# Performance work log

Measured on AMD Instinct MI355X. Metric: run time of the kernel, lower is better.

## Reference

```python
import jax, jax.numpy as jnp
import numpy as np

B, T, S, L, R, H, UE = 64, 256, 16, 128, 16, 256, 64


def setup_inputs() -> dict:
    key = jax.random.key(0)
    ks = jax.random.split(key, 10)
    u = jax.random.normal(ks[0], (B, T, UE), jnp.float32)
    k = 0.1 * jax.random.normal(ks[1], (B, T, L), jnp.float32)
    K = 0.1 * jax.random.normal(ks[2], (B, T, L, R), jnp.float32)
    eps_z = jax.random.normal(ks[3], (T, S, B, L), jnp.float32)
    eps_w = jax.random.normal(ks[4], (T, S, B, R), jnp.float32)
    W1 = jax.random.normal(ks[5], (L, H), jnp.float32) / np.sqrt(L).astype(np.float32)
    W2 = jax.random.normal(ks[6], (H, L), jnp.float32) / np.sqrt(H).astype(np.float32)
    m_init = jax.random.normal(ks[7], (L,), jnp.float32)
    Q_diag = jax.random.uniform(ks[8], (L,), jnp.float32, 0.1, 1.0)
    Q0_diag = jax.random.uniform(ks[9], (L,), jnp.float32, 0.5, 1.5)
    return dict(u=u, k=k, K=K, eps_z=eps_z, eps_w=eps_w, W1=W1, W2=W2,
                m_init=m_init, Q_diag=Q_diag, Q0_diag=Q0_diag, n_samples=S)


def reference(u, k, K, eps_z, eps_w, W1, W2, m_init, Q_diag, Q0_diag, n_samples):
    Bn, Tn, Ln, Rn = K.shape
    ue = u.shape[-1]
    I_r = jnp.eye(Rn, dtype=K.dtype)

    def bmv(A, x):      # A: [B,L,R], x: [...,B,R] -> [...,B,L]
        return jnp.einsum('blr,...br->...bl', A, x)

    def bmvT(A, x):     # A: [B,L,R], x: [...,B,L] -> [...,B,R]
        return jnp.einsum('blr,...bl->...br', A, x)

    def mean_fn(z):
        return z + jnp.tanh(z @ W1) @ W2

    def step_core(m, K_t, k_t, ez, ew, q_a):
        # A = I + K^T diag(q_a) K  (rank x rank)
        A = I_r + jnp.einsum('blr,l,blq->brq', K_t, q_a, K_t)
        Lc = jnp.linalg.cholesky(A)
        Linv = jax.scipy.linalg.solve_triangular(
            Lc, jnp.broadcast_to(I_r, Lc.shape), lower=True)

        def csolve(x):  # solve A y = x via Linv^T Linv x
            y = jnp.einsum('bij,...bj->...bi', Linv, x)
            return jnp.einsum('bji,...bj->...bi', Linv, y)

        # gain direction; inner shift always uses Q_diag (as in torch source)
        g = k_t - bmv(K_t, csolve(bmvT(K_t, m + Q_diag * k_t)))
        m_f = m + q_a * g
        z_p = jnp.sqrt(q_a) * ez
        z_f = m_f + z_p - bmv(K_t, csolve(bmvT(K_t, z_p) + ew))
        qp = jnp.sum(q_a * g * g, axis=-1)
        M = A - I_r  # = K^T diag(q_a) K
        tr = -jnp.einsum('bij,bjk,bik->b', Linv, M, Linv)
        logdet = 2.0 * jnp.sum(jnp.log(jnp.diagonal(Lc, axis1=-2, axis2=-1)), axis=-1)
        kl = 0.5 * (qp + tr + logdet)
        return z_f, m_f, z_p, kl

    # ---- t = 0 (uses initial covariance Q0_diag) ----
    m0 = jnp.broadcast_to(m_init, (Bn, Ln))
    m0 = m0.at[:, :ue].add(u[:, 0])
    z_f0, m_f0, z_p0, kl0 = step_core(m0, K[:, 0], k[:, 0], eps_z[0], eps_w[0], Q0_diag)

    # ---- t = 1..T-1: sequential nonlinear filter scan ----
    def scan_fn(z_prev, xs):
        u_t, k_t, K_t, ez, ew = xs
        m = mean_fn(z_prev)            # [S,B,L]
        m = m.at[..., :ue].add(u_t)    # broadcast input over samples
        z_f, m_f, z_p, kl = step_core(m, K_t, k_t, ez, ew, Q_diag)
        return z_f, (z_f, m_f.mean(axis=0), z_p, kl.mean(axis=0))

    xs = (jnp.swapaxes(u[:, 1:], 0, 1),
          jnp.swapaxes(k[:, 1:], 0, 1),
          jnp.swapaxes(K[:, 1:], 0, 1),
          eps_z[1:], eps_w[1:])
    _, (z_fs, m_fs, z_ps, kls) = jax.lax.scan(scan_fn, z_f0, xs)

    z_f = jnp.transpose(jnp.concatenate([z_f0[None], z_fs], 0), (1, 2, 0, 3))  # [S,B,T,L]
    m_f = jnp.transpose(jnp.concatenate([m_f0[None], m_fs], 0), (1, 0, 2))     # [B,T,L]
    z_p = jnp.transpose(jnp.concatenate([z_p0[None], z_ps], 0), (1, 2, 0, 3))  # [S,B,T,L]
    kl = jnp.concatenate([kl0[None], kls], 0).T                                 # [B,T]
    return z_f, m_f, z_p, kl
```

## Files before the change

kernel.cpp:

```cpp
#include <hip/hip_runtime.h>
#include <cstddef>

typedef _Float16 half8v __attribute__((ext_vector_type(8)));
typedef _Float16 half4v __attribute__((ext_vector_type(4)));
typedef float f32x4 __attribute__((ext_vector_type(4)));

#define MFMA32(A, B, C) __builtin_amdgcn_mfma_f32_16x16x32_f16(A, B, C, 0, 0, 0)
#define MFMA16(A, B, C) __builtin_amdgcn_mfma_f32_16x16x16f16(A, B, C, 0, 0, 0)

__global__ void kw2_kernel(const float* __restrict__ W2, _Float16* __restrict__ w2h) {
  int i = blockIdx.x * 256 + threadIdx.x;
  w2h[i] = (_Float16)W2[i];
}

__global__ void kprep1_kernel(const float* __restrict__ Kg,
                              const float* __restrict__ kg,
                              const float* __restrict__ ug,
                              const float* __restrict__ Qd,
                              const float* __restrict__ Q0d,
                              float* __restrict__ Ainv,
                              float* __restrict__ klc,
                              _Float16* __restrict__ pfb,
                              float* __restrict__ cgp) {
  int tid = threadIdx.x;
  int wv = tid >> 6, ln = tid & 63;
  size_t bt = (size_t)blockIdx.x * 4 + wv;
  int t = (int)(bt & 255);
  __shared__ float Ks[4][128][20];
  __shared__ float qs[4][128];
  __shared__ float vvs[4][128];
  __shared__ float Asm[4][16][20];
  __shared__ float LiL[4][16][20];
  __shared__ float AiS[4][16][20];
  __shared__ float yps[4][4][16];
  __shared__ float yvs[4][16];

  const float* kp = Kg + bt * 2048;
  for (int i = ln; i < 2048; i += 64) Ks[wv][i >> 4][i & 15] = kp[i];
  for (int l = ln; l < 128; l += 64) {
    float q = (t == 0) ? Q0d[l] : Qd[l];
    qs[wv][l] = q;
    float v = Qd[l] * kg[bt * 128 + l];
    if (t > 0 && l < 64) v += ug[bt * 64 + l];
    vvs[wv][l] = v;
  }
  __syncthreads();
  {
    int r = ln & 15, c0 = (ln >> 4) << 2;
    float a0 = 0, a1 = 0, a2 = 0, a3 = 0;
    for (int l = 0; l < 128; ++l) {
      float kq = Ks[wv][l][r] * qs[wv][l];
      const float* row = &Ks[wv][l][c0];
      a0 += kq * row[0]; a1 += kq * row[1]; a2 += kq * row[2]; a3 += kq * row[3];
    }
    Asm[wv][r][c0 + 0] = a0 + ((r == c0 + 0) ? 1.f : 0.f);
    Asm[wv][r][c0 + 1] = a1 + ((r == c0 + 1) ? 1.f : 0.f);
    Asm[wv][r][c0 + 2] = a2 + ((r == c0 + 2) ? 1.f : 0.f);
    Asm[wv][r][c0 + 3] = a3 + ((r == c0 + 3) ? 1.f : 0.f);
  }
  {
    int r = ln & 15, seg = ln >> 4;
    float s = 0.f;
    for (int l = seg * 32; l < seg * 32 + 32; ++l) s += Ks[wv][l][r] * vvs[wv][l];
    yps[wv][seg][r] = s;
  }
  __syncthreads();
  if (ln < 16) {
    int i = ln;
    float ar[16], Lr[16];
#pragma unroll
    for (int j = 0; j < 16; ++j) ar[j] = Asm[wv][i][j];
    float ld = 0.f;
#pragma unroll
    for (int j = 0; j < 16; ++j) {
      float ajj = __shfl(ar[j], j, 64);
      float d = sqrtf(ajj);
      ld += __logf(d);
      float li = ar[j] / d;
      li = (i >= j) ? li : 0.f;
      Lr[j] = li;
#pragma unroll
      for (int k2 = j; k2 < 16; ++k2) {
        float lk = __shfl(li, k2, 64);
        ar[k2] -= li * lk;
      }
    }
    int cc = i;
    float Lic[16];
#pragma unroll
    for (int ii = 0; ii < 16; ++ii) {
      float s = (ii == cc) ? 1.f : 0.f;
#pragma unroll
      for (int p = 0; p < 16; ++p) {
        if (p < ii) {
          float Lip = __shfl(Lr[p], ii, 64);
          s -= Lip * Lic[p];
        }
      }
      float dii = __shfl(Lr[ii], ii, 64);
      float v = s / dii;
      Lic[ii] = (ii >= cc) ? v : 0.f;
    }
    float tr = 0.f;
#pragma unroll
    for (int ii = 0; ii < 16; ++ii) { tr += Lic[ii] * Lic[ii]; LiL[wv][cc][ii] = Lic[ii]; }
    tr += __shfl_xor(tr, 1); tr += __shfl_xor(tr, 2);
    tr += __shfl_xor(tr, 4); tr += __shfl_xor(tr, 8);
    if (cc == 0) klc[bt] = 0.5f * (tr - 16.f + 2.f * ld);
    yvs[wv][cc] = yps[wv][0][cc] + yps[wv][1][cc] + yps[wv][2][cc] + yps[wv][3][cc];
  }
  __syncthreads();
  {
    int r = ln & 15, c0 = (ln >> 4) << 2;
    float a0 = 0, a1 = 0, a2 = 0, a3 = 0;
    for (int ii = 0; ii < 16; ++ii) {
      float lir = LiL[wv][r][ii];
      a0 += lir * LiL[wv][c0 + 0][ii];
      a1 += lir * LiL[wv][c0 + 1][ii];
      a2 += lir * LiL[wv][c0 + 2][ii];
      a3 += lir * LiL[wv][c0 + 3][ii];
    }
    AiS[wv][r][c0 + 0] = a0; AiS[wv][r][c0 + 1] = a1;
    AiS[wv][r][c0 + 2] = a2; AiS[wv][r][c0 + 3] = a3;
    f32x4 av = {a0, a1, a2, a3};
    *(f32x4*)&Ainv[bt * 256 + r * 16 + c0] = av;
  }
  __syncthreads();
  {
#pragma unroll
    for (int li = 0; li < 2; ++li) {
      int l = ln * 2 + li;
      f32x4 acc0 = {0,0,0,0}, acc1v = {0,0,0,0}, acc2v = {0,0,0,0}, acc3v = {0,0,0,0};
      for (int j = 0; j < 16; ++j) {
        float kj = Ks[wv][l][j];
        acc0  += kj * *(const f32x4*)&AiS[wv][j][0];
        acc1v += kj * *(const f32x4*)&AiS[wv][j][4];
        acc2v += kj * *(const f32x4*)&AiS[wv][j][8];
        acc3v += kj * *(const f32x4*)&AiS[wv][j][12];
      }
      float ql = qs[wv][l];
      float cp = ql * kg[bt * 128 + l];
      float pv[16];
#pragma unroll
      for (int e = 0; e < 4; ++e) {
        pv[e] = ql * acc0[e]; pv[4 + e] = ql * acc1v[e];
        pv[8 + e] = ql * acc2v[e]; pv[12 + e] = ql * acc3v[e];
      }
#pragma unroll
      for (int r = 0; r < 16; ++r) cp -= pv[r] * yvs[wv][r];
      cgp[bt * 128 + l] = cp;
#pragma unroll
      for (int r = 0; r < 16; ++r) Ks[wv][l][r] = pv[r];
    }
  }
  __syncthreads();
  {
    int gp = ln >> 4, cp = ln & 15;
#pragma unroll
    for (int ci = 0; ci < 4; ++ci) {
      half8v o;
#pragma unroll
      for (int mt = 0; mt < 2; ++mt)
#pragma unroll
        for (int j = 0; j < 4; ++j)
          o[mt * 4 + j] = (_Float16)Ks[wv][ci * 32 + mt * 16 + cp][gp * 4 + j];
      *(half8v*)(pfb + bt * 2048 + (size_t)(ci * 64 + ln) * 8) = o;
    }
  }
}

__global__ void kprepR_kernel(const float* __restrict__ Kg,
                              const _Float16* __restrict__ w2h,
                              _Float16* __restrict__ rfb,
                              _Float16* __restrict__ kab) {
  int tid = threadIdx.x;
  int wv = tid >> 6, ln = tid & 63;
  int g = ln >> 4, c = ln & 15;
  __shared__ _Float16 Kh[128][20];
  __shared__ _Float16 Rh[16][264];
  for (int it = 0; it < 4; ++it) {
    size_t bt = (size_t)blockIdx.x * 4 + it;
    const float* kp = Kg + bt * 2048;
    for (int i = tid; i < 2048; i += 256) Kh[i >> 4][i & 15] = (_Float16)kp[i];
    __syncthreads();
    half8v kA[4];
#pragma unroll
    for (int kt = 0; kt < 4; ++kt)
#pragma unroll
      for (int j = 0; j < 8; ++j) kA[kt][j] = Kh[kt * 32 + g * 8 + j][c];
#pragma unroll
    for (int i = 0; i < 4; ++i) {
      int tile = wv * 4 + i;
      f32x4 acc = {0, 0, 0, 0};
#pragma unroll
      for (int kt = 0; kt < 4; ++kt) {
        half8v bf = *(const half8v*)&w2h[(size_t)(tile * 16 + c) * 128 + kt * 32 + g * 8];
        acc = MFMA32(kA[kt], bf, acc);
      }
#pragma unroll
      for (int r = 0; r < 4; ++r) Rh[g * 4 + r][tile * 16 + c] = (_Float16)acc[r];
    }
    __syncthreads();
    half8v r0, r1;
#pragma unroll
    for (int mt = 0; mt < 4; ++mt)
#pragma unroll
      for (int j = 0; j < 4; ++j) {
        _Float16 v = Rh[c][wv * 64 + mt * 16 + g * 4 + j];
        if (mt < 2) r0[mt * 4 + j] = v; else r1[(mt - 2) * 4 + j] = v;
      }
    *(half8v*)(rfb + bt * 4096 + (size_t)tid * 16) = r0;
    *(half8v*)(rfb + bt * 4096 + (size_t)tid * 16 + 8) = r1;
    if (kab) {
      half8v ko;
#pragma unroll
      for (int kt = 0; kt < 2; ++kt)
#pragma unroll
        for (int j = 0; j < 4; ++j) ko[kt * 4 + j] = Kh[wv * 32 + kt * 16 + g * 4 + j][c];
      *(half8v*)(kab + bt * 2048 + (size_t)tid * 8) = ko;
    }
    __syncthreads();
  }
}

__global__ void kc_kernel(const float* __restrict__ Kg,
                          const float* __restrict__ epsz,
                          const float* __restrict__ epsw,
                          const float* __restrict__ Qd,
                          const float* __restrict__ Q0d,
                          const float* __restrict__ Ainv,
                          float* __restrict__ out_zf,
                          float* __restrict__ out_zp,
                          float* __restrict__ zpcb,
                          int zw, int wzp) {
  int idx = blockIdx.x;
  int t = idx >> 6, b = idx & 63;
  int bt = b * 256 + t;
  __shared__ float Ks[128][16];
  __shared__ float Ai[16][16];
  __shared__ float zp[16][129];
  __shared__ float hh[16][17];
  __shared__ float ww[16][17];
  __shared__ float sq[128];
  const float* kp = Kg + (size_t)bt * 2048;
  for (int i = threadIdx.x; i < 2048; i += 256) ((float*)Ks)[i] = kp[i];
  ((float*)Ai)[threadIdx.x] = Ainv[(size_t)bt * 256 + threadIdx.x];
  const float* q = (t == 0) ? Q0d : Qd;
  if (threadIdx.x < 128) sq[threadIdx.x] = sqrtf(q[threadIdx.x]);
  __syncthreads();
  for (int i = threadIdx.x; i < 2048; i += 256) {
    int s = i >> 7, l = i & 127;
    float v = sq[l] * epsz[(((size_t)t * 16 + s) * 64 + b) * 128 + l];
    zp[s][l] = v;
    if (wzp) out_zp[(((size_t)s * 64 + b) * 256 + t) * 128 + l] = v;
  }
  __syncthreads();
  {
    int s = threadIdx.x >> 4, r = threadIdx.x & 15;
    float acc = epsw[(((size_t)t * 16 + s) * 64 + b) * 16 + r];
    for (int l = 0; l < 128; ++l) acc += Ks[l][r] * zp[s][l];
    hh[s][r] = acc;
  }
  __syncthreads();
  {
    int s = threadIdx.x >> 4, r = threadIdx.x & 15;
    float acc = 0.f;
    for (int j = 0; j < 16; ++j) acc += Ai[r][j] * hh[s][j];
    ww[s][r] = acc;
  }
  __syncthreads();
  for (int i = threadIdx.x; i < 2048; i += 256) {
    int s = i >> 7, l = i & 127;
    float acc = 0.f;
    for (int r = 0; r < 16; ++r) acc += Ks[l][r] * ww[s][r];
    float v = zp[s][l] - acc;
    if (zw) zpcb[(size_t)bt * 2048 + i] = v;
    else out_zf[(((size_t)s * 64 + b) * 256 + t) * 128 + l] = v;
  }
}

__global__ void kzp_kernel(const float* __restrict__ epsz,
                           const float* __restrict__ Qd,
                           const float* __restrict__ Q0d,
                           float* __restrict__ out_zp) {
  for (size_t i = (size_t)blockIdx.x * blockDim.x + threadIdx.x; i < (size_t)33554432;
       i += (size_t)gridDim.x * blockDim.x) {
    int l = (int)(i & 127);
    int t = (int)((i >> 7) & 255);
    int sb = (int)(i >> 15);
    int s = sb >> 6, b = sb & 63;
    float q = (t == 0) ? Q0d[l] : Qd[l];
    out_zp[i] = sqrtf(q) * epsz[(((size_t)t * 16 + s) * 64 + b) * 128 + l];
  }
}

#define BAR() asm volatile("s_waitcnt lgkmcnt(0)\n\ts_barrier" ::: "memory")

template <bool PK, bool ZW>
__device__ __forceinline__ void scan_body(
    const int b, const int ct,
    _Float16* __restrict__ svhc, _Float16* __restrict__ hbc,
    float (*__restrict__ h2pc)[320], float (*__restrict__ qppc)[64],
    const float* __restrict__ ug, const float* __restrict__ Kg,
    const float* __restrict__ W1, const float* __restrict__ W2,
    const float* __restrict__ m_init, const float* __restrict__ Qd,
    const float* __restrict__ Q0d, const _Float16* __restrict__ pfb,
    const float* __restrict__ cgp, const _Float16* __restrict__ rfb,
    const _Float16* __restrict__ kab, const float* __restrict__ zpcb,
    const float* __restrict__ klcp, float* __restrict__ out_zf,
    float* __restrict__ out_mf, float* __restrict__ out_kl) {
  const int wvc = ct >> 6;
  const int ln = ct & 63;
  const int g = ln >> 4;
  const int c = ln & 15;

  half8v w1f[4][4];
#pragma unroll
  for (int mt = 0; mt < 4; ++mt)
#pragma unroll
    for (int kt = 0; kt < 4; ++kt) {
      half8v v;
#pragma unroll
      for (int j = 0; j < 8; ++j)
        v[j] = (_Float16)W1[(size_t)(kt * 32 + g * 8 + j) * 256 + (wvc * 64 + mt * 16 + c)];
      w1f[mt][kt] = v;
    }
  half8v w2f[2][8];
#pragma unroll
  for (int mt = 0; mt < 2; ++mt)
#pragma unroll
    for (int kt = 0; kt < 8; ++kt) {
      half8v v;
#pragma unroll
      for (int j = 0; j < 8; ++j)
        v[j] = (_Float16)W2[(size_t)(kt * 32 + g * 8 + j) * 128 + (wvc * 32 + mt * 16 + c)];
      w2f[mt][kt] = v;
    }

  f32x4 qiv[2], qiv0[2];
#pragma unroll
  for (int mt = 0; mt < 2; ++mt) {
    f32x4 q = *(const f32x4*)&Qd[wvc * 32 + mt * 16 + g * 4];
    f32x4 q0 = *(const f32x4*)&Q0d[wvc * 32 + mt * 16 + g * 4];
#pragma unroll
    for (int r = 0; r < 4; ++r) { qiv[mt][r] = 1.f / q[r]; qiv0[mt][r] = 1.f / q0[r]; }
  }

  f32x4 zreg[2];

  half8v pfx0, pfx1, kax0 = {}, kax1 = {}, rfa0, rfa1, rfc0, rfc1;
  float kf0[8], kf1[8];
  f32x4 zq0[2], zq1[2], cv0[2], cv1[2];
  f32x4 ur0[2] = {}, ur1[2] = {};
  float kv0 = 0.f, kv1 = 0.f;

  const char* pf_p = (const char*)pfb + (size_t)b * 256 * 4096 + (size_t)ct * 16;
  const char* ka_p = PK ? (const char*)kab + (size_t)b * 256 * 4096 + (size_t)ct * 16
                        : (const char*)pfb;
  const char* K_p = (const char*)Kg + (size_t)b * 256 * 8192 + (size_t)((wvc * 32 + g * 4) * 16 + c) * 4;
  const char* rf_p = (const char*)rfb + (size_t)b * 256 * 8192 + (size_t)ct * 32;
  const char* zq_p = ZW ? (const char*)zpcb + (size_t)b * 256 * 8192 + (size_t)(c * 128 + wvc * 32 + g * 4) * 4
                        : (const char*)out_zf + ((((size_t)c * 64 + b) * 256) * 128 + wvc * 32 + g * 4) * 4;
  const size_t zq_str = ZW ? 8192 : 512;
  const char* cv_p = (const char*)cgp + (size_t)b * 256 * 512 + (size_t)(wvc * 32 + g * 4) * 4;
  const char* ur_p = (const char*)ug + (size_t)b * 256 * 256 + (size_t)(wvc * 32 + g * 4) * 4;
  const char* kl_p = (const char*)klcp + (size_t)b * 256 * 4;
  char* zf_p = (char*)out_zf + ((((size_t)c * 64 + b) * 256) * 128 + wvc * 32 + g * 4) * 4;
  char* mf_p = (char*)out_mf + ((size_t)b * 256 * 128 + wvc * 32 + g * 4) * 4;

#define STAGE(BI) do { \
    pfx##BI = *(const half8v*)pf_p; pf_p += 4096; \
    if constexpr (PK) { kax##BI = *(const half8v*)ka_p; ka_p += 4096; } \
    else { _Pragma("unroll") for (int kt_ = 0; kt_ < 2; ++kt_) \
             _Pragma("unroll") for (int j_ = 0; j_ < 4; ++j_) \
               kf##BI[kt_ * 4 + j_] = *(const float*)(K_p + kt_ * 1024 + j_ * 64); \
           K_p += 8192; } \
// ... 113 lines not shown
      v_ += __shfl_xor(v_, 4); v_ += __shfl_xor(v_, 8); \
      if (ct == 0) out_kl[(size_t)b * 256 + (size_t)(TPREV)] = 0.03125f * v_ + kv##PBI; \
    } \
  } while (0)

  STAGE(0);
  STAGE(1);
  {
    f32x4 mv0[2];
#pragma unroll
    for (int mt = 0; mt < 2; ++mt) {
      mv0[mt] = *(const f32x4*)&m_init[wvc * 32 + mt * 16 + g * 4];
      if (wvc < 2) mv0[mt] += ur0[mt];
    }
    half4v mh0[2], ml0[2];
#pragma unroll
    for (int kt = 0; kt < 2; ++kt)
#pragma unroll
      for (int j = 0; j < 4; ++j) {
        float x = mv0[kt][j];
        _Float16 h = (_Float16)x;
        mh0[kt][j] = h;
        ml0[kt][j] = (_Float16)(x - (float)h);
      }
    half4v ka0_, ka1_;
    KAH(0, 0, ka0_); KAH(0, 1, ka1_);
    f32x4 hz = {0, 0, 0, 0};
    hz = MFMA16(ka0_, mh0[0], hz); hz = MFMA16(ka1_, mh0[1], hz);
    hz = MFMA16(ka0_, ml0[0], hz); hz = MFMA16(ka1_, ml0[1], hz);
    *(f32x4*)&h2pc[wvc][c * 20 + g * 4] = hz;
    BAR();
    EPILOG(0, qiv0, mv0);
    BAR();
  }

  for (int t = 1; t < 255; t += 2) {
    KL_FIN(0, t - 1);
    STAGE(0);
    PHASE_A(1);
    BAR();
    PHASE_B(1, qiv);
    BAR();
    KL_FIN(1, t);
    STAGE(1);
    PHASE_A(0);
    BAR();
    PHASE_B(0, qiv);
    BAR();
  }
  KL_FIN(0, 254);
  PHASE_A(1);
  BAR();
  PHASE_B(1, qiv);
  BAR();
  KL_FIN(1, 255);

#undef STAGE
#undef KAH
#undef PHASE_A
#undef EPILOG
#undef PHASE_B
#undef KL_FIN
}

template <bool PK, bool ZW>
__launch_bounds__(256, 1)
__global__ void kscan1_kernel(const float* __restrict__ ug, const float* __restrict__ Kg,
                              const float* __restrict__ W1, const float* __restrict__ W2,
                              const float* __restrict__ m_init, const float* __restrict__ Qd,
                              const float* __restrict__ Q0d, const _Float16* __restrict__ pfb,
                              const float* __restrict__ cgp, const _Float16* __restrict__ rfb,
                              const _Float16* __restrict__ kab, const float* __restrict__ zpcb,
                              const float* __restrict__ klcp, float* __restrict__ out_zf,
                              float* __restrict__ out_mf, float* __restrict__ out_kl) {
  __shared__ __align__(16) _Float16 svh[2048];
  __shared__ __align__(16) _Float16 hb[4096];
  __shared__ float h2p[4][320];
  __shared__ float qpp[2][64];
  scan_body<PK, ZW>(blockIdx.x, threadIdx.x, svh, hb, h2p, qpp,
                    ug, Kg, W1, W2, m_init, Qd, Q0d, pfb, cgp, rfb, kab, zpcb, klcp,
                    out_zf, out_mf, out_kl);
}

template <bool PK, bool ZW>
__attribute__((amdgpu_flat_work_group_size(512, 512)))
__attribute__((amdgpu_waves_per_eu(2, 2)))
__global__ void kscan2_kernel(const float* __restrict__ ug, const float* __restrict__ Kg,
                              const float* __restrict__ W1, const float* __restrict__ W2,
                              const float* __restrict__ m_init, const float* __restrict__ Qd,
                              const float* __restrict__ Q0d, const _Float16* __restrict__ pfb,
                              const float* __restrict__ cgp, const _Float16* __restrict__ rfb,
                              const _Float16* __restrict__ kab, const float* __restrict__ zpcb,
                              const float* __restrict__ klcp, float* __restrict__ out_zf,
                              float* __restrict__ out_mf, float* __restrict__ out_kl) {
  __shared__ __align__(16) _Float16 svh[2][2048];
  __shared__ __align__(16) _Float16 hb[2][4096];
  __shared__ float h2p[2][4][320];
  __shared__ float qpp[2][2][64];
  const int ch = threadIdx.x >> 8;
  scan_body<PK, ZW>(blockIdx.x * 2 + ch, threadIdx.x & 255,
                    svh[ch], hb[ch], h2p[ch], qpp[ch],
                    ug, Kg, W1, W2, m_init, Qd, Q0d, pfb, cgp, rfb, kab, zpcb, klcp,
                    out_zf, out_mf, out_kl);
}

extern "C" void kernel_launch(void* const* d_in, const int* in_sizes, int n_in,
                              void* d_out, int out_size, void* d_ws, size_t ws_size,
                              hipStream_t stream) {
  (void)in_sizes; (void)n_in; (void)out_size;
  const float* u   = (const float*)d_in[0];
  const float* kk  = (const float*)d_in[1];
  const float* Kg  = (const float*)d_in[2];
  const float* epz = (const float*)d_in[3];
  const float* epw = (const float*)d_in[4];
  const float* W1  = (const float*)d_in[5];
  const float* W2  = (const float*)d_in[6];
  const float* mi  = (const float*)d_in[7];
  const float* Qd  = (const float*)d_in[8];
  const float* Q0d = (const float*)d_in[9];

  float* out_zf = (float*)d_out;
  float* out_mf = out_zf + (size_t)33554432;
  float* out_zp = out_mf + (size_t)2097152;
  float* out_kl = out_zp + (size_t)33554432;

  char* ws = (char*)d_ws;
  size_t off = 0;
  auto take = [&](size_t n) { char* p = ws + off; off += n; return p; };
  float*    Ainv = (float*)take(16777216);
  float*    klc  = (float*)take(65536);
  float*    cgp  = (float*)take(8388608);
  _Float16* pfb  = (_Float16*)take(67108864);
  _Float16* w2h  = (_Float16*)take(65536);
  bool zw = ws_size >= off + 134217728;
  float* zpcb = zw ? (float*)take(134217728) : nullptr;
  bool pk = zw && (ws_size >= off + 67108864);
  _Float16* kab = pk ? (_Float16*)take(67108864) : nullptr;
  bool rfws = ws_size >= off + 134217728;
  _Float16* rfb = rfws ? (_Float16*)take(134217728) : (_Float16*)out_zp;
  int wzp = rfws ? 1 : 0;

  kw2_kernel<<<128, 256, 0, stream>>>(W2, w2h);
  kprep1_kernel<<<4096, 256, 0, stream>>>(Kg, kk, u, Qd, Q0d, Ainv, klc, pfb, cgp);
  kprepR_kernel<<<4096, 256, 0, stream>>>(Kg, w2h, rfb, kab);
  kc_kernel<<<16384, 256, 0, stream>>>(Kg, epz, epw, Qd, Q0d, Ainv, out_zf, out_zp,
                                       zpcb, zw ? 1 : 0, wzp);

  auto pick = [&](const void* f2) {
    hipFuncAttributes fa;
    if (hipFuncGetAttributes(&fa, f2) == hipSuccess)
      return fa.localSizeBytes == 0 && fa.numRegs > 140;
    return false;
  };
#define LAUNCH_SCAN(PKV, ZWV) do { \
    if (pick((const void*)kscan2_kernel<PKV, ZWV>)) \
      kscan2_kernel<PKV, ZWV><<<32, 512, 0, stream>>>(u, Kg, W1, W2, mi, Qd, Q0d, pfb, cgp, rfb, kab, zpcb, klc, out_zf, out_mf, out_kl); \
    else \
      kscan1_kernel<PKV, ZWV><<<64, 256, 0, stream>>>(u, Kg, W1, W2, mi, Qd, Q0d, pfb, cgp, rfb, kab, zpcb, klc, out_zf, out_mf, out_kl); \
  } while (0)

  if (pk)      LAUNCH_SCAN(true,  true);
  else if (zw) LAUNCH_SCAN(false, true);
  else         LAUNCH_SCAN(false, false);
#undef LAUNCH_SCAN

  if (!rfws) kzp_kernel<<<2048, 256, 0, stream>>>(epz, Qd, Q0d, out_zp);
}
```

Before: 1.078 ms.

## Fuse R-factor precompute into correction kernel and drop two-chain scan variant

Adds a kc2 kernel that computes the fp16 K·W2 R-factors and fp16 K copy inside the same per-(b,t) block that computes the noise correction, so K is read from global memory once instead of twice. Introduces a fixed workspace layout path when the workspace is large enough, always writing z_p directly and launching the single-chain kscan1 scan. Removes the runtime attribute-based selection of the 512-thread two-chain scan kernel. The trade-off is a heavier fused kernel with more shared memory and fewer parallel blocks per CU, plus losing the kscan2 variant if it was the one being picked.

```diff
diff --git a/kernel.cpp b/kernel.cpp
--- a/kernel.cpp
+++ b/kernel.cpp
@@ -11,287 +11,6 @@
 __global__ void kw2_kernel(const float* __restrict__ W2, _Float16* __restrict__ w2h) {
   int i = blockIdx.x * 256 + threadIdx.x;
   w2h[i] = (_Float16)W2[i];
-}
-
-__global__ void kprep1_kernel(const float* __restrict__ Kg,
-                              const float* __restrict__ kg,
-                              const float* __restrict__ ug,
-                              const float* __restrict__ Qd,
-                              const float* __restrict__ Q0d,
-                              float* __restrict__ Ainv,
-                              float* __restrict__ klc,
-                              _Float16* __restrict__ pfb,
-                              float* __restrict__ cgp) {
-  int tid = threadIdx.x;
-  int wv = tid >> 6, ln = tid & 63;
-  size_t bt = (size_t)blockIdx.x * 4 + wv;
-  int t = (int)(bt & 255);
-  __shared__ float Ks[4][128][20];
-  __shared__ float qs[4][128];
-  __shared__ float vvs[4][128];
-  __shared__ float Asm[4][16][20];
-  __shared__ float LiL[4][16][20];
-  __shared__ float AiS[4][16][20];
-  __shared__ float yps[4][4][16];
-  __shared__ float yvs[4][16];
-
-  const float* kp = Kg + bt * 2048;
-  for (int i = ln; i < 2048; i += 64) Ks[wv][i >> 4][i & 15] = kp[i];
-  for (int l = ln; l < 128; l += 64) {
-    float q = (t == 0) ? Q0d[l] : Qd[l];
-    qs[wv][l] = q;
-    float v = Qd[l] * kg[bt * 128 + l];
-    if (t > 0 && l < 64) v += ug[bt * 64 + l];
-    vvs[wv][l] = v;
-  }
-  __syncthreads();
-  {
-    int r = ln & 15, c0 = (ln >> 4) << 2;
-    float a0 = 0, a1 = 0, a2 = 0, a3 = 0;
-    for (int l = 0; l < 128; ++l) {
-      float kq = Ks[wv][l][r] * qs[wv][l];
-      const float* row = &Ks[wv][l][c0];
-      a0 += kq * row[0]; a1 += kq * row[1]; a2 += kq * row[2]; a3 += kq * row[3];
-    }
-    Asm[wv][r][c0 + 0] = a0 + ((r == c0 + 0) ? 1.f : 0.f);
-    Asm[wv][r][c0 + 1] = a1 + ((r == c0 + 1) ? 1.f : 0.f);
-    Asm[wv][r][c0 + 2] = a2 + ((r == c0 + 2) ? 1.f : 0.f);
-    Asm[wv][r][c0 + 3] = a3 + ((r == c0 + 3) ? 1.f : 0.f);
-  }
-  {
-    int r = ln & 15, seg = ln >> 4;
-    float s = 0.f;
-    for (int l = seg * 32; l < seg * 32 + 32; ++l) s += Ks[wv][l][r] * vvs[wv][l];
-    yps[wv][seg][r] = s;
-  }
-  __syncthreads();
-  if (ln < 16) {
-    int i = ln;
-    float ar[16], Lr[16];
-#pragma unroll
-    for (int j = 0; j < 16; ++j) ar[j] = Asm[wv][i][j];
-    float ld = 0.f;
-#pragma unroll
-    for (int j = 0; j < 16; ++j) {
-      float ajj = __shfl(ar[j], j, 64);
-      float d = sqrtf(ajj);
-      ld += __logf(d);
-      float li = ar[j] / d;
-      li = (i >= j) ? li : 0.f;
-      Lr[j] = li;
-#pragma unroll
-      for (int k2 = j; k2 < 16; ++k2) {
-        float lk = __shfl(li, k2, 64);
-        ar[k2] -= li * lk;
-      }
-    }
-    int cc = i;
-    float Lic[16];
-#pragma unroll
-    for (int ii = 0; ii < 16; ++ii) {
-      float s = (ii == cc) ? 1.f : 0.f;
-#pragma unroll
-      for (int p = 0; p < 16; ++p) {
-        if (p < ii) {
-          float Lip = __shfl(Lr[p], ii, 64);
-          s -= Lip * Lic[p];
-        }
-      }
-      float dii = __shfl(Lr[ii], ii, 64);
-      float v = s / dii;
-      Lic[ii] = (ii >= cc) ? v : 0.f;
-    }
-    float tr = 0.f;
-#pragma unroll
-    for (int ii = 0; ii < 16; ++ii) { tr += Lic[ii] * Lic[ii]; LiL[wv][cc][ii] = Lic[ii]; }
-    tr += __shfl_xor(tr, 1); tr += __shfl_xor(tr, 2);
-    tr += __shfl_xor(tr, 4); tr += __shfl_xor(tr, 8);
-    if (cc == 0) klc[bt] = 0.5f * (tr - 16.f + 2.f * ld);
-    yvs[wv][cc] = yps[wv][0][cc] + yps[wv][1][cc] + yps[wv][2][cc] + yps[wv][3][cc];
-  }
-  __syncthreads();
-  {
-    int r = ln & 15, c0 = (ln >> 4) << 2;
-    float a0 = 0, a1 = 0, a2 = 0, a3 = 0;
-    for (int ii = 0; ii < 16; ++ii) {
-      float lir = LiL[wv][r][ii];
-      a0 += lir * LiL[wv][c0 + 0][ii];
-      a1 += lir * LiL[wv][c0 + 1][ii];
-      a2 += lir * LiL[wv][c0 + 2][ii];
-      a3 += lir * LiL[wv][c0 + 3][ii];
-    }
-    AiS[wv][r][c0 + 0] = a0; AiS[wv][r][c0 + 1] = a1;
-    AiS[wv][r][c0 + 2] = a2; AiS[wv][r][c0 + 3] = a3;
-    f32x4 av = {a0, a1, a2, a3};
-    *(f32x4*)&Ainv[bt * 256 + r * 16 + c0] = av;
-  }
-  __syncthreads();
-  {
-#pragma unroll
-    for (int li = 0; li < 2; ++li) {
-      int l = ln * 2 + li;
-      f32x4 acc0 = {0,0,0,0}, acc1v = {0,0,0,0}, acc2v = {0,0,0,0}, acc3v = {0,0,0,0};
-      for (int j = 0; j < 16; ++j) {
-        float kj = Ks[wv][l][j];
-        acc0  += kj * *(const f32x4*)&AiS[wv][j][0];
-        acc1v += kj * *(const f32x4*)&AiS[wv][j][4];
-        acc2v += kj * *(const f32x4*)&AiS[wv][j][8];
-        acc3v += kj * *(const f32x4*)&AiS[wv][j][12];
-      }
-      float ql = qs[wv][l];
-      float cp = ql * kg[bt * 128 + l];
-      float pv[16];
-#pragma unroll
-      for (int e = 0; e < 4; ++e) {
-        pv[e] = ql * acc0[e]; pv[4 + e] = ql * acc1v[e];
-        pv[8 + e] = ql * acc2v[e]; pv[12 + e] = ql * acc3v[e];
-      }
-#pragma unroll
-      for (int r = 0; r < 16; ++r) cp -= pv[r] * yvs[wv][r];
-      cgp[bt * 128 + l] = cp;
-#pragma unroll
-      for (int r = 0; r < 16; ++r) Ks[wv][l][r] = pv[r];
-    }
-  }
-  __syncthreads();
-  {
-    int gp = ln >> 4, cp = ln & 15;
-#pragma unroll
-    for (int ci = 0; ci < 4; ++ci) {
-      half8v o;
-#pragma unroll
-      for (int mt = 0; mt < 2; ++mt)
-#pragma unroll
-        for (int j = 0; j < 4; ++j)
-          o[mt * 4 + j] = (_Float16)Ks[wv][ci * 32 + mt * 16 + cp][gp * 4 + j];
-      *(half8v*)(pfb + bt * 2048 + (size_t)(ci * 64 + ln) * 8) = o;
-    }
-  }
-}
-
-__global__ void kprepR_kernel(const float* __restrict__ Kg,
-                              const _Float16* __restrict__ w2h,
-                              _Float16* __restrict__ rfb,
-                              _Float16* __restrict__ kab) {
-  int tid = threadIdx.x;
-  int wv = tid >> 6, ln = tid & 63;
-  int g = ln >> 4, c = ln & 15;
-  __shared__ _Float16 Kh[128][20];
-  __shared__ _Float16 Rh[16][264];
-  for (int it = 0; it < 4; ++it) {
-    size_t bt = (size_t)blockIdx.x * 4 + it;
-    const float* kp = Kg + bt * 2048;
-    for (int i = tid; i < 2048; i += 256) Kh[i >> 4][i & 15] = (_Float16)kp[i];
-    __syncthreads();
-    half8v kA[4];
-#pragma unroll
-    for (int kt = 0; kt < 4; ++kt)
-#pragma unroll
-      for (int j = 0; j < 8; ++j) kA[kt][j] = Kh[kt * 32 + g * 8 + j][c];
-#pragma unroll
-    for (int i = 0; i < 4; ++i) {
-      int tile = wv * 4 + i;
-      f32x4 acc = {0, 0, 0, 0};
-#pragma unroll
-      for (int kt = 0; kt < 4; ++kt) {
-        half8v bf = *(const half8v*)&w2h[(size_t)(tile * 16 + c) * 128 + kt * 32 + g * 8];
-        acc = MFMA32(kA[kt], bf, acc);
-      }
-#pragma unroll
-      for (int r = 0; r < 4; ++r) Rh[g * 4 + r][tile * 16 + c] = (_Float16)acc[r];
-    }
-    __syncthreads();
-    half8v r0, r1;
-#pragma unroll
-    for (int mt = 0; mt < 4; ++mt)
-#pragma unroll
-      for (int j = 0; j < 4; ++j) {
-        _Float16 v = Rh[c][wv * 64 + mt * 16 + g * 4 + j];
-        if (mt < 2) r0[mt * 4 + j] = v; else r1[(mt - 2) * 4 + j] = v;
-      }
-    *(half8v*)(rfb + bt * 4096 + (size_t)tid * 16) = r0;
-    *(half8v*)(rfb + bt * 4096 + (size_t)tid * 16 + 8) = r1;
-    if (kab) {
-      half8v ko;
-#pragma unroll
-      for (int kt = 0; kt < 2; ++kt)
-#pragma unroll
-        for (int j = 0; j < 4; ++j) ko[kt * 4 + j] = Kh[wv * 32 + kt * 16 + g * 4 + j][c];
-      *(half8v*)(kab + bt * 2048 + (size_t)tid * 8) = ko;
-    }
-    __syncthreads();
-  }
-}
-
-__global__ void kc_kernel(const float* __restrict__ Kg,
-                          const float* __restrict__ epsz,
-                          const float* __restrict__ epsw,
-                          const float* __restrict__ Qd,
-                          const float* __restrict__ Q0d,
-                          const float* __restrict__ Ainv,
-                          float* __restrict__ out_zf,
-                          float* __restrict__ out_zp,
-                          float* __restrict__ zpcb,
-                          int zw, int wzp) {
-  int idx = blockIdx.x;
-  int t = idx >> 6, b = idx & 63;
-  int bt = b * 256 + t;
-  __shared__ float Ks[128][16];
-  __shared__ float Ai[16][16];
-  __shared__ float zp[16][129];
-  __shared__ float hh[16][17];
-  __shared__ float ww[16][17];
-  __shared__ float sq[128];
-  const float* kp = Kg + (size_t)bt * 2048;
-  for (int i = threadIdx.x; i < 2048; i += 256) ((float*)Ks)[i] = kp[i];
-  ((float*)Ai)[threadIdx.x] = Ainv[(size_t)bt * 256 + threadIdx.x];
-  const float* q = (t == 0) ? Q0d : Qd;
-  if (threadIdx.x < 128) sq[threadIdx.x] = sqrtf(q[threadIdx.x]);
-  __syncthreads();
-  for (int i = threadIdx.x; i < 2048; i += 256) {
-    int s = i >> 7, l = i & 127;
-    float v = sq[l] * epsz[(((size_t)t * 16 + s) * 64 + b) * 128 + l];
-    zp[s][l] = v;
-    if (wzp) out_zp[(((size_t)s * 64 + b) * 256 + t) * 128 + l] = v;
-  }
-  __syncthreads();
-  {
-    int s = threadIdx.x >> 4, r = threadIdx.x & 15;
-    float acc = epsw[(((size_t)t * 16 + s) * 64 + b) * 16 + r];
-    for (int l = 0; l < 128; ++l) acc += Ks[l][r] * zp[s][l];
-    hh[s][r] = acc;
-  }
-  __syncthreads();
-  {
-    int s = threadIdx.x >> 4, r = threadIdx.x & 15;
-    float acc = 0.f;
-    for (int j = 0; j < 16; ++j) acc += Ai[r][j] * hh[s][j];
-    ww[s][r] = acc;
-  }
-  __syncthreads();
-  for (int i = threadIdx.x; i < 2048; i += 256) {
-    int s = i >> 7, l = i & 127;
-    float acc = 0.f;
-    for (int r = 0; r < 16; ++r) acc += Ks[l][r] * ww[s][r];
-    float v = zp[s][l] - acc;
-    if (zw) zpcb[(size_t)bt * 2048 + i] = v;
-    else out_zf[(((size_t)s * 64 + b) * 256 + t) * 128 + l] = v;
-  }
-}
-
-__global__ void kzp_kernel(const float* __restrict__ epsz,
-                           const float* __restrict__ Qd,
-                           const float* __restrict__ Q0d,
-                           float* __restrict__ out_zp) {
-  for (size_t i = (size_t)blockIdx.x * blockDim.x + threadIdx.x; i < (size_t)33554432;
-       i += (size_t)gridDim.x * blockDim.x) {
-    int l = (int)(i & 127);
-    int t = (int)((i >> 7) & 255);
-    int sb = (int)(i >> 15);
-    int s = sb >> 6, b = sb & 63;
-    float q = (t == 0) ? Q0d[l] : Qd[l];
-    out_zp[i] = sqrtf(q) * epsz[(((size_t)t * 16 + s) * 64 + b) * 128 + l];
-  }
 }
 
 #define BAR() asm volatile("s_waitcnt lgkmcnt(0)\n\ts_barrier" ::: "memory")
@@ -571,26 +290,361 @@
                     out_zf, out_mf, out_kl);
 }
 
-template <bool PK, bool ZW>
-__attribute__((amdgpu_flat_work_group_size(512, 512)))
-__attribute__((amdgpu_waves_per_eu(2, 2)))
-__global__ void kscan2_kernel(const float* __restrict__ ug, const float* __restrict__ Kg,
-                              const float* __restrict__ W1, const float* __restrict__ W2,
-                              const float* __restrict__ m_init, const float* __restrict__ Qd,
-                              const float* __restrict__ Q0d, const _Float16* __restrict__ pfb,
-                              const float* __restrict__ cgp, const _Float16* __restrict__ rfb,
-                              const _Float16* __restrict__ kab, const float* __restrict__ zpcb,
-                              const float* __restrict__ klcp, float* __restrict__ out_zf,
-                              float* __restrict__ out_mf, float* __restrict__ out_kl) {
-  __shared__ __align__(16) _Float16 svh[2][2048];
-  __shared__ __align__(16) _Float16 hb[2][4096];
-  __shared__ float h2p[2][4][320];
-  __shared__ float qpp[2][2][64];
-  const int ch = threadIdx.x >> 8;
-  scan_body<PK, ZW>(blockIdx.x * 2 + ch, threadIdx.x & 255,
-                    svh[ch], hb[ch], h2p[ch], qpp[ch],
-                    ug, Kg, W1, W2, m_init, Qd, Q0d, pfb, cgp, rfb, kab, zpcb, klcp,
-                    out_zf, out_mf, out_kl);
+__global__ void kprep1_kernel(const float* __restrict__ Kg, const float* __restrict__ kg,
+                              const float* __restrict__ ug, const float* __restrict__ Qd,
+                              const float* __restrict__ Q0d, float* __restrict__ Ainv,
+                              float* __restrict__ klc, _Float16* __restrict__ pfb,
+                              float* __restrict__ cgp) {
+  int tid = threadIdx.x;
+  int wv = tid >> 6, ln = tid & 63;
+  size_t bt = (size_t)blockIdx.x * 4 + wv;
+  int t = (int)(bt & 255);
+  __shared__ float Ks[4][128][20];
+  __shared__ float qs[4][128];
+  __shared__ float vvs[4][128];
+  __shared__ float Asm[4][16][20];
+  __shared__ float LiL[4][16][20];
+  __shared__ float AiS[4][16][20];
+  __shared__ float yps[4][4][16];
+  __shared__ float yvs[4][16];
+  const float* kp = Kg + bt * 2048;
+  for (int i = ln; i < 2048; i += 64) Ks[wv][i >> 4][i & 15] = kp[i];
+  for (int l = ln; l < 128; l += 64) {
+    float q = (t == 0) ? Q0d[l] : Qd[l];
+    qs[wv][l] = q;
+    float v = Qd[l] * kg[bt * 128 + l];
+    if (t > 0 && l < 64) v += ug[bt * 64 + l];
+    vvs[wv][l] = v;
+  }
+  __syncthreads();
+  {
+    int r = ln & 15, c0 = (ln >> 4) << 2;
+    float a0 = 0, a1 = 0, a2 = 0, a3 = 0;
+    for (int l = 0; l < 128; ++l) {
+      float kq = Ks[wv][l][r] * qs[wv][l];
+      const float* row = &Ks[wv][l][c0];
+      a0 += kq * row[0]; a1 += kq * row[1]; a2 += kq * row[2]; a3 += kq * row[3];
+    }
+    Asm[wv][r][c0 + 0] = a0 + ((r == c0 + 0) ? 1.f : 0.f);
+    Asm[wv][r][c0 + 1] = a1 + ((r == c0 + 1) ? 1.f : 0.f);
+    Asm[wv][r][c0 + 2] = a2 + ((r == c0 + 2) ? 1.f : 0.f);
+    Asm[wv][r][c0 + 3] = a3 + ((r == c0 + 3) ? 1.f : 0.f);
+  }
+  {
+    int r = ln & 15, seg = ln >> 4;
+    float s = 0.f;
+    for (int l = seg * 32; l < seg * 32 + 32; ++l) s += Ks[wv][l][r] * vvs[wv][l];
+    yps[wv][seg][r] = s;
+  }
+  __syncthreads();
+  if (ln < 16) {
+    int i = ln;
+    float ar[16], Lr[16];
+#pragma unroll
+    for (int j = 0; j < 16; ++j) ar[j] = Asm[wv][i][j];
+    float ld = 0.f;
+#pragma unroll
+    for (int j = 0; j < 16; ++j) {
+      float ajj = __shfl(ar[j], j, 64);
+      float d = sqrtf(ajj);
+      ld += __logf(d);
+      float li = ar[j] / d;
+      li = (i >= j) ? li : 0.f;
+      Lr[j] = li;
+#pragma unroll
+      for (int k2 = j; k2 < 16; ++k2) {
+        float lk = __shfl(li, k2, 64);
+        ar[k2] -= li * lk;
+      }
+    }
+    int cc = i;
+    float Lic[16];
+#pragma unroll
+    for (int ii = 0; ii < 16; ++ii) {
+      float s = (ii == cc) ? 1.f : 0.f;
+#pragma unroll
+      for (int p = 0; p < 16; ++p) {
+        if (p < ii) {
+          float Lip = __shfl(Lr[p], ii, 64);
+          s -= Lip * Lic[p];
+        }
+      }
+      float dii = __shfl(Lr[ii], ii, 64);
+      float v = s / dii;
+      Lic[ii] = (ii >= cc) ? v : 0.f;
+    }
+    float tr = 0.f;
+#pragma unroll
+    for (int ii = 0; ii < 16; ++ii) { tr += Lic[ii] * Lic[ii]; LiL[wv][cc][ii] = Lic[ii]; }
+    tr += __shfl_xor(tr, 1); tr += __shfl_xor(tr, 2);
+    tr += __shfl_xor(tr, 4); tr += __shfl_xor(tr, 8);
+    if (cc == 0) klc[bt] = 0.5f * (tr - 16.f + 2.f * ld);
+    yvs[wv][cc] = yps[wv][0][cc] + yps[wv][1][cc] + yps[wv][2][cc] + yps[wv][3][cc];
+  }
+  __syncthreads();
+  {
+    int r = ln & 15, c0 = (ln >> 4) << 2;
+    float a0 = 0, a1 = 0, a2 = 0, a3 = 0;
+    for (int ii = 0; ii < 16; ++ii) {
+      float lir = LiL[wv][r][ii];
+      a0 += lir * LiL[wv][c0 + 0][ii];
+      a1 += lir * LiL[wv][c0 + 1][ii];
+      a2 += lir * LiL[wv][c0 + 2][ii];
+      a3 += lir * LiL[wv][c0 + 3][ii];
+    }
+    AiS[wv][r][c0 + 0] = a0; AiS[wv][r][c0 + 1] = a1;
+    AiS[wv][r][c0 + 2] = a2; AiS[wv][r][c0 + 3] = a3;
+    f32x4 av = {a0, a1, a2, a3};
+    *(f32x4*)&Ainv[bt * 256 + r * 16 + c0] = av;
+  }
+  __syncthreads();
+  {
+#pragma unroll
+    for (int li = 0; li < 2; ++li) {
+      int l = ln * 2 + li;
+      f32x4 acc0 = {0,0,0,0}, acc1v = {0,0,0,0}, acc2v = {0,0,0,0}, acc3v = {0,0,0,0};
+      for (int j = 0; j < 16; ++j) {
+        float kj = Ks[wv][l][j];
+        acc0  += kj * *(const f32x4*)&AiS[wv][j][0];
+        acc1v += kj * *(const f32x4*)&AiS[wv][j][4];
+        acc2v += kj * *(const f32x4*)&AiS[wv][j][8];
+        acc3v += kj * *(const f32x4*)&AiS[wv][j][12];
+      }
+      float ql = qs[wv][l];
+      float cp = ql * kg[bt * 128 + l];
+      float pv[16];
+#pragma unroll
+      for (int e = 0; e < 4; ++e) {
+        pv[e] = ql * acc0[e]; pv[4 + e] = ql * acc1v[e];
+        pv[8 + e] = ql * acc2v[e]; pv[12 + e] = ql * acc3v[e];
+      }
+#pragma unroll
+      for (int r = 0; r < 16; ++r) cp -= pv[r] * yvs[wv][r];
+      cgp[bt * 128 + l] = cp;
+#pragma unroll
+      for (int r = 0; r < 16; ++r) Ks[wv][l][r] = pv[r];
+    }
+  }
+  __syncthreads();
+  {
+    int gp = ln >> 4, cp = ln & 15;
+#pragma unroll
+    for (int ci = 0; ci < 4; ++ci) {
+      half8v o;
+#pragma unroll
+      for (int mt = 0; mt < 2; ++mt)
+#pragma unroll
+        for (int j = 0; j < 4; ++j)
+          o[mt * 4 + j] = (_Float16)Ks[wv][ci * 32 + mt * 16 + cp][gp * 4 + j];
+      *(half8v*)(pfb + bt * 2048 + (size_t)(ci * 64 + ln) * 8) = o;
+    }
+  }
+}
+
+__global__ void kc2_kernel(const float* __restrict__ Kg, const float* __restrict__ epsz,
+                           const float* __restrict__ epsw, const float* __restrict__ Qd,
+                           const float* __restrict__ Q0d, const float* __restrict__ Ainv,
+                           const _Float16* __restrict__ w2h,
+                           _Float16* __restrict__ rfb, _Float16* __restrict__ kab,
+                           float* __restrict__ zpcb, float* __restrict__ out_zp) {
+  int idx = blockIdx.x;
+  int t = idx >> 6, b = idx & 63;
+  size_t bt = (size_t)b * 256 + t;
+  int tid = threadIdx.x;
+  const int wv = tid >> 6, ln = tid & 63, g = ln >> 4, c = ln & 15;
+  __shared__ float Ks[128][17];
+  __shared__ float Ai[16][16];
+  __shared__ float zp[16][129];
+  __shared__ float hh[16][17];
+  __shared__ float ww[16][17];
+  __shared__ float sq[128];
+  __shared__ _Float16 Rh[16][264];
+  const float* kp = Kg + bt * 2048;
+  for (int i = tid; i < 2048; i += 256) Ks[i >> 4][i & 15] = kp[i];
+  ((float*)Ai)[tid] = Ainv[bt * 256 + tid];
+  const float* q = (t == 0) ? Q0d : Qd;
+  if (tid < 128) sq[tid] = sqrtf(q[tid]);
+  __syncthreads();
+  for (int i = tid; i < 2048; i += 256) {
+    int s = i >> 7, l = i & 127;
+    float v = sq[l] * epsz[(((size_t)t * 16 + s) * 64 + b) * 128 + l];
+    zp[s][l] = v;
+    out_zp[(((size_t)s * 64 + b) * 256 + t) * 128 + l] = v;
+  }
+  {
+    half8v kA[4];
+#pragma unroll
+    for (int kt = 0; kt < 4; ++kt)
+#pragma unroll
+      for (int j = 0; j < 8; ++j) kA[kt][j] = (_Float16)Ks[kt * 32 + g * 8 + j][c];
+#pragma unroll
+    for (int i = 0; i < 4; ++i) {
+      int tile = wv * 4 + i;
+      f32x4 acc = {0, 0, 0, 0};
+#pragma unroll
+      for (int kt = 0; kt < 4; ++kt) {
+        half8v bf = *(const half8v*)&w2h[(size_t)(tile * 16 + c) * 128 + kt * 32 + g * 8];
+        acc = MFMA32(kA[kt], bf, acc);
+      }
+#pragma unroll
+      for (int r = 0; r < 4; ++r) Rh[g * 4 + r][tile * 16 + c] = (_Float16)acc[r];
+    }
+  }
+  __syncthreads();
+  {
+    int s = tid >> 4, r = tid & 15;
+    float acc = epsw[(((size_t)t * 16 + s) * 64 + b) * 16 + r];
+    for (int l = 0; l < 128; ++l) acc += Ks[l][r] * zp[s][l];
+    hh[s][r] = acc;
+  }
+  {
+    half8v r0, r1;
+#pragma unroll
+    for (int mt = 0; mt < 4; ++mt)
+#pragma unroll
+      for (int j = 0; j < 4; ++j) {
+        _Float16 v = Rh[c][wv * 64 + mt * 16 + g * 4 + j];
+        if (mt < 2) r0[mt * 4 + j] = v; else r1[(mt - 2) * 4 + j] = v;
+      }
+    *(half8v*)(rfb + bt * 4096 + (size_t)tid * 16) = r0;
+    *(half8v*)(rfb + bt * 4096 + (size_t)tid * 16 + 8) = r1;
+    half8v ko;
+#pragma unroll
+    for (int kt = 0; kt < 2; ++kt)
+#pragma unroll
+      for (int j = 0; j < 4; ++j) ko[kt * 4 + j] = (_Float16)Ks[wv * 32 + kt * 16 + g * 4 + j][c];
+    *(half8v*)(kab + bt * 2048 + (size_t)tid * 8) = ko;
+  }
+  __syncthreads();
+  {
+    int s = tid >> 4, r = tid & 15;
+    float acc = 0.f;
+    for (int j = 0; j < 16; ++j) acc += Ai[r][j] * hh[s][j];
+    ww[s][r] = acc;
+  }
+  __syncthreads();
+  for (int i = tid; i < 2048; i += 256) {
+    int s = i >> 7, l = i & 127;
+    float acc = 0.f;
+    for (int r = 0; r < 16; ++r) acc += Ks[l][r] * ww[s][r];
+    zpcb[bt * 2048 + i] = zp[s][l] - acc;
+  }
+}
+
+__global__ void kprepR_kernel(const float* __restrict__ Kg, const _Float16* __restrict__ w2h,
+                              _Float16* __restrict__ rfb, _Float16* __restrict__ kab) {
+  int tid = threadIdx.x;
+  int wv = tid >> 6, ln = tid & 63;
+  int g = ln >> 4, c = ln & 15;
+  __shared__ _Float16 Kh[128][20];
+  __shared__ _Float16 Rh[16][264];
+  for (int it = 0; it < 4; ++it) {
+    size_t bt = (size_t)blockIdx.x * 4 + it;
+    const float* kp = Kg + bt * 2048;
+    for (int i = tid; i < 2048; i += 256) Kh[i >> 4][i & 15] = (_Float16)kp[i];
+    __syncthreads();
+    half8v kA[4];
+#pragma unroll
+    for (int kt = 0; kt < 4; ++kt)
+#pragma unroll
+      for (int j = 0; j < 8; ++j) kA[kt][j] = Kh[kt * 32 + g * 8 + j][c];
+#pragma unroll
+    for (int i = 0; i < 4; ++i) {
+      int tile = wv * 4 + i;
+      f32x4 acc = {0, 0, 0, 0};
+#pragma unroll
+      for (int kt = 0; kt < 4; ++kt) {
+        half8v bf = *(const half8v*)&w2h[(size_t)(tile * 16 + c) * 128 + kt * 32 + g * 8];
+        acc = MFMA32(kA[kt], bf, acc);
+      }
+#pragma unroll
+      for (int r = 0; r < 4; ++r) Rh[g * 4 + r][tile * 16 + c] = (_Float16)acc[r];
+    }
+    __syncthreads();
+    half8v r0, r1;
+#pragma unroll
+    for (int mt = 0; mt < 4; ++mt)
+#pragma unroll
+      for (int j = 0; j < 4; ++j) {
+        _Float16 v = Rh[c][wv * 64 + mt * 16 + g * 4 + j];
+        if (mt < 2) r0[mt * 4 + j] = v; else r1[(mt - 2) * 4 + j] = v;
+      }
+    *(half8v*)(rfb + bt * 4096 + (size_t)tid * 16) = r0;
+    *(half8v*)(rfb + bt * 4096 + (size_t)tid * 16 + 8) = r1;
+    if (kab) {
+      half8v ko;
+#pragma unroll
+      for (int kt = 0; kt < 2; ++kt)
+#pragma unroll
+        for (int j = 0; j < 4; ++j) ko[kt * 4 + j] = Kh[wv * 32 + kt * 16 + g * 4 + j][c];
+      *(half8v*)(kab + bt * 2048 + (size_t)tid * 8) = ko;
+    }
+    __syncthreads();
+  }
+}
+
+__global__ void kc_kernel(const float* __restrict__ Kg, const float* __restrict__ epsz,
+                          const float* __restrict__ epsw, const float* __restrict__ Qd,
+                          const float* __restrict__ Q0d, const float* __restrict__ Ainv,
+                          float* __restrict__ out_zf, float* __restrict__ out_zp,
+                          float* __restrict__ zpcb, int zw, int wzp) {
+  int idx = blockIdx.x;
+  int t = idx >> 6, b = idx & 63;
+  int bt = b * 256 + t;
+  __shared__ float Ks[128][16];
+  __shared__ float Ai[16][16];
+  __shared__ float zp[16][129];
+  __shared__ float hh[16][17];
+  __shared__ float ww[16][17];
+  __shared__ float sq[128];
+  const float* kp = Kg + (size_t)bt * 2048;
+  for (int i = threadIdx.x; i < 2048; i += 256) ((float*)Ks)[i] = kp[i];
+  ((float*)Ai)[threadIdx.x] = Ainv[(size_t)bt * 256 + threadIdx.x];
+  const float* q = (t == 0) ? Q0d : Qd;
+  if (threadIdx.x < 128) sq[threadIdx.x] = sqrtf(q[threadIdx.x]);
+  __syncthreads();
+  for (int i = threadIdx.x; i < 2048; i += 256) {
+    int s = i >> 7, l = i & 127;
+    float v = sq[l] * epsz[(((size_t)t * 16 + s) * 64 + b) * 128 + l];
+    zp[s][l] = v;
+    if (wzp) out_zp[(((size_t)s * 64 + b) * 256 + t) * 128 + l] = v;
+  }
+  __syncthreads();
+  {
+    int s = threadIdx.x >> 4, r = threadIdx.x & 15;
+    float acc = epsw[(((size_t)t * 16 + s) * 64 + b) * 16 + r];
+    for (int l = 0; l < 128; ++l) acc += Ks[l][r] * zp[s][l];
+    hh[s][r] = acc;
+  }
+  __syncthreads();
+  {
+    int s = threadIdx.x >> 4, r = threadIdx.x & 15;
+    float acc = 0.f;
+    for (int j = 0; j < 16; ++j) acc += Ai[r][j] * hh[s][j];
+    ww[s][r] = acc;
+  }
+  __syncthreads();
+  for (int i = threadIdx.x; i < 2048; i += 256) {
+    int s = i >> 7, l = i & 127;
+    float acc = 0.f;
+    for (int r = 0; r < 16; ++r) acc += Ks[l][r] * ww[s][r];
+    float v = zp[s][l] - acc;
+    if (zw) zpcb[(size_t)bt * 2048 + i] = v;
+    else out_zf[(((size_t)s * 64 + b) * 256 + t) * 128 + l] = v;
+  }
+}
+
+__global__ void kzp_kernel(const float* __restrict__ epsz, const float* __restrict__ Qd,
+                           const float* __restrict__ Q0d, float* __restrict__ out_zp) {
+  for (size_t i = (size_t)blockIdx.x * blockDim.x + threadIdx.x; i < (size_t)33554432;
+       i += (size_t)gridDim.x * blockDim.x) {
+    int l = (int)(i & 127);
+    int t = (int)((i >> 7) & 255);
+    int sb = (int)(i >> 15);
+    int s = sb >> 6, b = sb & 63;
+    float q = (t == 0) ? Q0d[l] : Qd[l];
+    out_zp[i] = sqrtf(q) * epsz[(((size_t)t * 16 + s) * 64 + b) * 128 + l];
+  }
 }
 
 extern "C" void kernel_launch(void* const* d_in, const int* in_sizes, int n_in,
@@ -614,6 +668,36 @@
   float* out_kl = out_zp + (size_t)33554432;
 
   char* ws = (char*)d_ws;
+
+  const size_t F_klc  = 0;
+  const size_t F_cgp  = 65536;
+  const size_t F_pfb  = 8454144;
+  const size_t F_w2h  = 75563008;
+  const size_t F_kab  = 75628544;
+  const size_t F_rfb  = 142737408;
+  const size_t F_zpc  = 276955136;
+  const size_t F_ainv = 411172864;
+  const size_t F_END  = 427950080;
+
+  if (ws_size >= F_END) {
+    float*    klc  = (float*)(ws + F_klc);
+    float*    cgp  = (float*)(ws + F_cgp);
+    _Float16* pfb  = (_Float16*)(ws + F_pfb);
+    _Float16* w2h  = (_Float16*)(ws + F_w2h);
+    _Float16* kab  = (_Float16*)(ws + F_kab);
+    _Float16* rfb  = (_Float16*)(ws + F_rfb);
+    float*    zpcb = (float*)(ws + F_zpc);
+    float*    Ainv = (float*)(ws + F_ainv);
+    kw2_kernel<<<128, 256, 0, stream>>>(W2, w2h);
+    kprep1_kernel<<<4096, 256, 0, stream>>>(Kg, kk, u, Qd, Q0d, Ainv, klc, pfb, cgp);
+    kc2_kernel<<<16384, 256, 0, stream>>>(Kg, epz, epw, Qd, Q0d, Ainv, w2h,
+                                          rfb, kab, zpcb, out_zp);
+    kscan1_kernel<true, true><<<64, 256, 0, stream>>>(u, Kg, W1, W2, mi, Qd, Q0d, pfb,
+                                                      cgp, rfb, kab, zpcb, klc,
+                                                      out_zf, out_mf, out_kl);
+    return;
+  }
+
   size_t off = 0;
   auto take = [&](size_t n) { char* p = ws + off; off += n; return p; };
   float*    Ainv = (float*)take(16777216);
@@ -634,24 +718,11 @@
   kprepR_kernel<<<4096, 256, 0, stream>>>(Kg, w2h, rfb, kab);
   kc_kernel<<<16384, 256, 0, stream>>>(Kg, epz, epw, Qd, Q0d, Ainv, out_zf, out_zp,
                                        zpcb, zw ? 1 : 0, wzp);
-
-  auto pick = [&](const void* f2) {
-    hipFuncAttributes fa;
-    if (hipFuncGetAttributes(&fa, f2) == hipSuccess)
-      return fa.localSizeBytes == 0 && fa.numRegs > 140;
-    return false;
-  };
-#define LAUNCH_SCAN(PKV, ZWV) do { \
-    if (pick((const void*)kscan2_kernel<PKV, ZWV>)) \
-      kscan2_kernel<PKV, ZWV><<<32, 512, 0, stream>>>(u, Kg, W1, W2, mi, Qd, Q0d, pfb, cgp, rfb, kab, zpcb, klc, out_zf, out_mf, out_kl); \
-    else \
-      kscan1_kernel<PKV, ZWV><<<64, 256, 0, stream>>>(u, Kg, W1, W2, mi, Qd, Q0d, pfb, cgp, rfb, kab, zpcb, klc, out_zf, out_mf, out_kl); \
-  } while (0)
-
-  if (pk)      LAUNCH_SCAN(true,  true);
-  else if (zw) LAUNCH_SCAN(false, true);
-  else         LAUNCH_SCAN(false, false);
-#undef LAUNCH_SCAN
-
+  if (pk)
+    kscan1_kernel<true, true><<<64, 256, 0, stream>>>(u, Kg, W1, W2, mi, Qd, Q0d, pfb, cgp, rfb, kab, zpcb, klc, out_zf, out_mf, out_kl);
+  else if (zw)
+    kscan1_kernel<false, true><<<64, 256, 0, stream>>>(u, Kg, W1, W2, mi, Qd, Q0d, pfb, cgp, rfb, kab, zpcb, klc, out_zf, out_mf, out_kl);
+  else
+    kscan1_kernel<false, false><<<64, 256, 0, stream>>>(u, Kg, W1, W2, mi, Qd, Q0d, pfb, cgp, rfb, kab, zpcb, klc, out_zf, out_mf, out_kl);
   if (!rfws) kzp_kernel<<<2048, 256, 0, stream>>>(epz, Qd, Q0d, out_zp);
 }
```

New measurement: 1.032 ms. -4.3%, faster.
